# Performance work log

Measured on AMD Instinct MI355X. Metric: run time of the kernel, lower is better.

The kernel has to match this reference:

```python
import jax, jax.numpy as jnp
import numpy as np

D = 128            # actual_dim
DM = 2 * D         # d_model = 256
DI = 2 * DM        # support-encoder inner dim = 512
H = 2 * DM         # LSTMCell hidden = 512
NUM_SYMBOLS = 200000
KNN_K = 10
PROCESS_STEPS = 4
BQ, BS, NN = 4096, 128, 64


def setup_inputs() -> dict:
    key = jax.random.key(0)
    ks = jax.random.split(key, 20)
    ri = lambda k, shape, hi: jax.random.randint(k, shape, 0, hi)
    rn = lambda k, shape, s=0.05: jax.random.normal(k, shape, jnp.float32) * s
    emb = rn(ks[0], (NUM_SYMBOLS + 1, D), 0.1).at[NUM_SYMBOLS].set(0.0)  # padding row
    return {
        "query": ri(ks[1], (BQ, 2), NUM_SYMBOLS),
        "support": ri(ks[2], (BS, 2), NUM_SYMBOLS),
        "q_l_conn": ri(ks[3], (BQ, NN, 2), NUM_SYMBOLS),
        "q_l_deg": ri(ks[4], (BQ,), NN),
        "q_r_conn": ri(ks[5], (BQ, NN, 2), NUM_SYMBOLS),
        "q_r_deg": ri(ks[6], (BQ,), NN),
        "s_l_conn": ri(ks[7], (BS, NN, 2), NUM_SYMBOLS),
        "s_l_deg": ri(ks[8], (BS,), NN),
        "s_r_conn": ri(ks[9], (BS, NN, 2), NUM_SYMBOLS),
        "s_r_deg": ri(ks[10], (BS,), NN),
        "emb": emb,
        "gcn_W": rn(ks[11], (D, 2 * D)),
        "gcn_wb": jnp.zeros((D,), jnp.float32),
        "gcn_b": jnp.zeros((D,), jnp.float32),
        "se_w1": rn(ks[12], (DI, DM)),
        "se_b1": jnp.zeros((DI,), jnp.float32),
        "se_w2": rn(ks[13], (DM, DI)),
        "se_b2": jnp.zeros((DM,), jnp.float32),
        "ln_g": jnp.ones((DM,), jnp.float32),
        "ln_b": jnp.zeros((DM,), jnp.float32),
        "W_ih": rn(ks[14], (4 * H, DM)),
        "W_hh": rn(ks[15], (4 * H, H)),
        "b_ih": jnp.zeros((4 * H,), jnp.float32),
        "b_hh": jnp.zeros((4 * H,), jnp.float32),
    }


def _cos(a, b, eps=1e-8):
    num = jnp.sum(a * b, -1)
    den = jnp.maximum(jnp.linalg.norm(a, axis=-1), eps) * jnp.maximum(jnp.linalg.norm(b, axis=-1), eps)
    return num / den


def _neighbor_encoder(emb, gcn_W, gcn_wb, gcn_b, conn, ent_ids):
    rel = emb[conn[..., 0]]                     # [B,N,D]
    ent = emb[conn[..., 1]]                     # [B,N,D]
    center = emb[ent_ids][:, None, :]           # [B,1,D]
    sim = _cos(center, ent)                     # [B,N]
    _, idx = jax.lax.top_k(sim, KNN_K)          # [B,K]
    rel_k = jnp.take_along_axis(rel, idx[..., None], axis=1)
    ent_k = jnp.take_along_axis(ent, idx[..., None], axis=1)
    cat = jnp.concatenate([rel_k, ent_k], -1)   # [B,K,2D]
    h = jnp.einsum('bkf,df->bkd', cat, gcn_W) + gcn_wb + gcn_b
    return jnp.tanh(h.mean(axis=1))             # [B,D]


def _support_encoder(x, w1, b1, w2, b2, g, b):
    # residual FFN + LayerNorm (GMatching SupportEncoder), dropout off (eval)
    out = jax.nn.relu(x @ w1.T + b1) @ w2.T + b2
    y = out + x
    mu = y.mean(-1, keepdims=True)
    var = ((y - mu) ** 2).mean(-1, keepdims=True)
    return (y - mu) / jnp.sqrt(var + 1e-5) * g + b


def _query_encoder(support, query, W_ih, W_hh, b_ih, b_hh):
    # GMatching attentive LSTM process block. support: [1,DM], query: [B,DM]
    B = query.shape[0]
    h_r = jnp.zeros((B, H), query.dtype)
    c = jnp.zeros((B, H), query.dtype)
    h = query
    for _ in range(PROCESS_STEPS):
        gates = query @ W_ih.T + b_ih + h_r @ W_hh.T + b_hh
        i, f, g_, o = jnp.split(gates, 4, axis=-1)  # torch LSTMCell gate order
        c = jax.nn.sigmoid(f) * c + jax.nn.sigmoid(i) * jnp.tanh(g_)
        h_new = jax.nn.sigmoid(o) * jnp.tanh(c)     # [B,H]
        h = query + h_new[:, :DM]                   # [B,DM]
        attn = jax.nn.softmax(h @ support.T, axis=1)  # [B,1]
        r = attn @ support                          # [B,DM]
        h_r = jnp.concatenate([h, r], axis=1)       # [B,H]
    return h


def reference(query, support, q_l_conn, q_l_deg, q_r_conn, q_r_deg,
              s_l_conn, s_l_deg, s_r_conn, s_r_deg,
              emb, gcn_W, gcn_wb, gcn_b,
              se_w1, se_b1, se_w2, se_b2, ln_g, ln_b,
              W_ih, W_hh, b_ih, b_hh):
    ne = lambda conn, ids: _neighbor_encoder(emb, gcn_W, gcn_wb, gcn_b, conn, ids)
    q_nb = jnp.concatenate([ne(q_l_conn, query[:, 0]), ne(q_r_conn, query[:, 1])], -1)    # [BQ,DM]
    s_nb = jnp.concatenate([ne(s_l_conn, support[:, 0]), ne(s_r_conn, support[:, 1])], -1)  # [BS,DM]
    se = lambda x: _support_encoder(x, se_w1, se_b1, se_w2, se_b2, ln_g, ln_b)
    support_g = se(s_nb).mean(axis=0, keepdims=True)  # [1,DM]
    query_g = se(q_nb)                                # [BQ,DM]
    qf = _query_encoder(support_g, query_g, W_ih, W_hh, b_ih, b_hh)
    l2 = lambda x: x / jnp.maximum(jnp.linalg.norm(x, axis=-1, keepdims=True), 1e-12)
    return (l2(qf) @ l2(support_g).T).squeeze(-1)     # [BQ]
```

## Files before the change

kernel.cpp:

```cpp
#include <hip/hip_runtime.h>
#include <hip/hip_bf16.h>

#define D   128
#define DM  256
#define DI  512
#define HH  512
#define KNN 10
#define NN  64
#define BQ  4096
#define BS  128
#define BM2 (BQ + BS)
#define G2  1024
#define GK  256
#define NSYM 200000
#define NEB (BQ * 2 + BS * 2)
#define BKT 64
#define LDP (BKT + 8)

__device__ __forceinline__ float sigmoidf_(float x) {
    return 1.f / (1.f + __expf(-x));
}
__device__ __forceinline__ float tanh_fast(float x) {
    x = fminf(fmaxf(x, -20.f), 20.f);
    float e = __expf(2.f * x);
    return (e - 1.f) / (e + 1.f);
}
__device__ __forceinline__ ushort f2bf(float x) {
    union { float f; unsigned u; } v; v.f = x;
    unsigned r = (v.u + 0x7fffu + ((v.u >> 16) & 1u)) >> 16;
    return (ushort)r;
}

typedef __bf16  bf16x8  __attribute__((ext_vector_type(8)));
typedef float   floatx4 __attribute__((ext_vector_type(4)));

__global__ __launch_bounds__(256) void ne_prep_kernel(
    const int* __restrict__ q_l, const int* __restrict__ q_r,
    const int* __restrict__ q_ids,
    const int* __restrict__ s_l, const int* __restrict__ s_r,
    const int* __restrict__ s_ids,
    const float* __restrict__ emb,
    float* __restrict__ catm_out,
    const float* __restrict__ W_ih, const float* __restrict__ W_hh,
    const float* __restrict__ b_ih, const float* __restrict__ b_hh,
    const float* __restrict__ se_w1, const float* __restrict__ se_w2,
    ushort* __restrict__ wih_bf, ushort* __restrict__ whh_bf,
    float* __restrict__ bsumP, ushort* __restrict__ w1_bf,
    ushort* __restrict__ w2_bf)
{
    int bid = blockIdx.x;
    int tid = threadIdx.x;

    if (bid >= NEB) {
        int pb = bid - NEB;
        if (pb < G2) {
            int n = pb;
            int bn = n >> 7, r = n & 127;
            int half = (r >> 6) & 1, j = (r >> 4) & 3, l = r & 15;
            int u = bn * 32 + half * 16 + l;
            int oldrow = j * 512 + u;
            wih_bf[n * 256 + tid] = f2bf(W_ih[(size_t)oldrow * DM + tid]);
            whh_bf[n * 256 + tid] = f2bf(W_hh[(size_t)oldrow * HH + tid]);
            if (tid == 0) bsumP[n] = b_ih[oldrow] + b_hh[oldrow];
        } else {
            int idx = (pb - G2) * 256 + tid;
            w1_bf[idx] = f2bf(se_w1[idx]);
            w2_bf[idx] = f2bf(se_w2[idx]);
        }
        return;
    }

    const int *conn_l, *conn_r, *ids;
    int row;
    if (bid < BQ * 2) { conn_l = q_l; conn_r = q_r; ids = q_ids; row = bid >> 1; }
    else { conn_l = s_l; conn_r = s_r; ids = s_ids; row = (bid - BQ * 2) >> 1; }
    int side = bid & 1;
    const int* conn = (side ? conn_r : conn_l) + (size_t)row * NN * 2;
    int cid = ids[row * 2 + side];

    __shared__ int   connb[NN * 2];
    __shared__ float sim[NN];
    __shared__ int   selr[KNN], sele[KNN];

    int wave = tid >> 6, lane = tid & 63;
    int grp = lane >> 4, l16 = lane & 15;

    if (tid < NN * 2) connb[tid] = conn[tid];
    const float* cp = &emb[(size_t)cid * D + l16 * 8];
    float4 c4a = *(const float4*)cp;
    float4 c4b = *(const float4*)(cp + 4);
    float cs = c4a.x * c4a.x + c4a.y * c4a.y + c4a.z * c4a.z + c4a.w * c4a.w
             + c4b.x * c4b.x + c4b.y * c4b.y + c4b.z * c4b.z + c4b.w * c4b.w;
    #pragma unroll
    for (int off = 8; off; off >>= 1) cs += __shfl_xor(cs, off);
    float cnorm = fmaxf(sqrtf(cs), 1e-8f);
    __syncthreads();

    float4 ea[4], eb[4];
    #pragma unroll
    for (int b = 0; b < 4; b++) {
        int j = wave * 16 + b * 4 + grp;
        int eid = connb[j * 2 + 1];
        const float* ep = &emb[(size_t)eid * D + l16 * 8];
        ea[b] = *(const float4*)ep;
        eb[b] = *(const float4*)(ep + 4);
    }
    #pragma unroll
    for (int b = 0; b < 4; b++) {
        int j = wave * 16 + b * 4 + grp;
        float dot = c4a.x * ea[b].x + c4a.y * ea[b].y + c4a.z * ea[b].z + c4a.w * ea[b].w
                  + c4b.x * eb[b].x + c4b.y * eb[b].y + c4b.z * eb[b].z + c4b.w * eb[b].w;
        float ee  = ea[b].x * ea[b].x + ea[b].y * ea[b].y + ea[b].z * ea[b].z + ea[b].w * ea[b].w
                  + eb[b].x * eb[b].x + eb[b].y * eb[b].y + eb[b].z * eb[b].z + eb[b].w * eb[b].w;
        #pragma unroll
        for (int off = 8; off; off >>= 1) {
            dot += __shfl_xor(dot, off);
            ee  += __shfl_xor(ee, off);
        }
        if (l16 == 0) sim[j] = dot / (cnorm * fmaxf(sqrtf(ee), 1e-8f));
    }
    __syncthreads();

    if (wave == 0) {
        float s = sim[lane];
        int id = lane;
        for (int k = 0; k < KNN; k++) {
            float bs = s; int bi = id;
            #pragma unroll
            for (int off = 32; off; off >>= 1) {
                float os = __shfl_xor(bs, off);
                int   oi = __shfl_xor(bi, off);
                if (os > bs || (os == bs && oi < bi)) { bs = os; bi = oi; }
            }
            if (lane == 0) { selr[k] = connb[bi * 2]; sele[k] = connb[bi * 2 + 1]; }
            if (id == bi) s = -__builtin_inff();
        }
    }
    __syncthreads();

    float acc = 0.f;
    if (tid < D) {
        #pragma unroll
        for (int k = 0; k < KNN; k++) acc += emb[(size_t)selr[k] * D + tid];
    } else {
        int d = tid - D;
        #pragma unroll
        for (int k = 0; k < KNN; k++) acc += emb[(size_t)sele[k] * D + d];
    }
    catm_out[(size_t)bid * DM + tid] = acc * (1.f / KNN);
}

#define GR 16
__global__ __launch_bounds__(256) void gcn_kernel(
    const float* __restrict__ catm, const float* __restrict__ gcn_W,
    const float* __restrict__ gcn_wb, const float* __restrict__ gcn_b,
    float* __restrict__ out, ushort* __restrict__ out_bf)
{
    __shared__ float cs[GR][DM];
    __shared__ float pp[GR][DM];
    int tid = threadIdx.x;
    int m0 = blockIdx.x * GR;
    #pragma unroll
    for (int t = 0; t < 4; t++) {
        int chunk = tid + 256 * t;
        int r = chunk >> 6, c4 = chunk & 63;
        *(float4*)&cs[r][c4 * 4] = *(const float4*)&catm[(size_t)(m0 + r) * DM + c4 * 4];
    }
    __syncthreads();

    int d = tid & 127, half = tid >> 7;
    float a[GR];
    #pragma unroll
    for (int r = 0; r < GR; r++) a[r] = 0.f;
    const float4* W4 = (const float4*)(gcn_W + (size_t)d * DM + half * D);
    for (int f4 = 0; f4 < D / 4; ++f4) {
        float4 w = W4[f4];
        #pragma unroll
        for (int r = 0; r < GR; r++) {
            const float* c = &cs[r][half * D + f4 * 4];
            a[r] += w.x * c[0] + w.y * c[1] + w.z * c[2] + w.w * c[3];
        }
    }
    #pragma unroll
    for (int r = 0; r < GR; r++) pp[r][tid] = a[r];
    __syncthreads();
    if (tid < D) {
        #pragma unroll
        for (int r = 0; r < GR; r++) {
            float h = pp[r][tid] + pp[r][tid + D] + gcn_wb[tid] + gcn_b[tid];
            float th = tanh_fast(h);
            out[(size_t)(m0 + r) * D + tid] = th;
            out_bf[(size_t)(m0 + r) * D + tid] = f2bf(th);
        }
    }
}

#define GEMM64_VARS()                                                         \
    __shared__ __align__(16) ushort As[64][LDP];                              \
    __shared__ __align__(16) ushort Bs[128][LDP];                             \
    int tid = threadIdx.x;                                                    \
    int wave = tid >> 6, lane = tid & 63;                                     \
    int quad = lane >> 4, l16 = lane & 15;                                    \
    int wm = (wave >> 1) * 32, wn = (wave & 1) * 64;

#define GEMM64_CORE(AP, BP, KDIM)                                             \
    floatx4 acc[2][4];                                                        \
    _Pragma("unroll")                                                         \
    for (int i = 0; i < 2; i++)                                               \
        _Pragma("unroll")                                                     \
        for (int j = 0; j < 4; j++) acc[i][j] = (floatx4){0.f, 0.f, 0.f, 0.f};\
    for (int k0 = 0; k0 < (KDIM); k0 += BKT) {                                \
        __syncthreads();                                                      \
        _Pragma("unroll")                                                     \
        for (int t = 0; t < 2; t++) {                                         \
            int ch = t * 256 + tid;                                           \
            int r = ch >> 3, c8 = (ch & 7) * 8;                               \
            *(uint4*)&As[r][c8] = *(const uint4*)&(AP)[(size_t)(bm * 64 + r) * (KDIM) + k0 + c8]; \
        }                                                                     \
        _Pragma("unroll")                                                     \
        for (int t = 0; t < 4; t++) {                                         \
            int ch = t * 256 + tid;                                           \
            int r = ch >> 3, c8 = (ch & 7) * 8;                               \
            *(uint4*)&Bs[r][c8] = *(const uint4*)&(BP)[(size_t)(bn * 128 + r) * (KDIM) + k0 + c8]; \
        }                                                                     \
        __syncthreads();                                                      \
        _Pragma("unroll")                                                     \
        for (int kk = 0; kk < BKT; kk += 32) {                                \
            bf16x8 af[2], bv[4];                                              \
            _Pragma("unroll")                                                 \
            for (int i = 0; i < 2; i++)                                       \
                af[i] = *(const bf16x8*)&As[wm + i * 16 + l16][kk + quad * 8];\
            _Pragma("unroll")                                                 \
            for (int j = 0; j < 4; j++)                                       \
                bv[j] = *(const bf16x8*)&Bs[wn + j * 16 + l16][kk + quad * 8];\
            _Pragma("unroll")                                                 \
            for (int i = 0; i < 2; i++)                                       \
                _Pragma("unroll")                                             \
                for (int j = 0; j < 4; j++)                                   \
                    acc[i][j] = __builtin_amdgcn_mfma_f32_16x16x32_bf16(      \
                        af[i], bv[j], acc[i][j], 0, 0, 0);                    \
        }                                                                     \
    }

__global__ __launch_bounds__(256) void se_gemm1_kernel(
    const ushort* __restrict__ A, const ushort* __restrict__ B,
    const float* __restrict__ b1, ushort* __restrict__ Cbf)
{
    GEMM64_VARS();
    int bm = blockIdx.x, bn = blockIdx.y;
    GEMM64_CORE(A, B, DM);
    #pragma unroll
    for (int i = 0; i < 2; i++) {
        #pragma unroll
        for (int j = 0; j < 4; j++) {
            int row = bm * 64 + wm + i * 16 + quad * 4;
            int col = bn * 128 + wn + j * 16 + l16;
            float bb = b1[col];
            #pragma unroll
            for (int rr = 0; rr < 4; rr++)
                Cbf[(size_t)(row + rr) * DI + col] = f2bf(fmaxf(acc[i][j][rr] + bb, 0.f));
        }
    }
}

__global__ __launch_bounds__(256) void se_gemm2_kernel(
    const ushort* __restrict__ A, const ushort* __restrict__ B,
    const float* __restrict__ b2, const float* __restrict__ xres,
    float* __restrict__ C)
{
    GEMM64_VARS();
    int bm = blockIdx.x, bn = blockIdx.y;
    GEMM64_CORE(A, B, DI);
    #pragma unroll
    for (int i = 0; i < 2; i++) {
        #pragma unroll
        for (int j = 0; j < 4; j++) {
            int row = bm * 64 + wm + i * 16 + quad * 4;
            int col = bn * 128 + wn + j * 16 + l16;
            float bb = b2[col];
            #pragma unroll
            for (int rr = 0; rr < 4; rr++)
                C[(size_t)(row + rr) * DM + col] =
                    acc[i][j][rr] + bb + xres[(size_t)(row + rr) * DM + col];
        }
    }
}

#define LN_ROWS 8
__global__ __launch_bounds__(256) void ln_kernel(
    const float* __restrict__ ys, const float* __restrict__ g,
    const float* __restrict__ b, float* __restrict__ outf,
    ushort* __restrict__ outbf)
{
    int tid = threadIdx.x;
    int wave = tid >> 6, lane = tid & 63;
    int r0 = blockIdx.x * LN_ROWS;
    for (int rr = 0; rr < 2; ++rr) {
        int r = r0 + wave * 2 + rr;
        float vals[4];
        float s = 0.f;
        #pragma unroll
        for (int e = 0; e < 4; e++) {
            vals[e] = ys[(size_t)r * DM + e * 64 + lane];
            s += vals[e];
        }
        #pragma unroll
        for (int off = 32; off; off >>= 1) s += __shfl_xor(s, off);
        float mu = s * (1.f / DM);
        float v = 0.f;
        #pragma unroll
        for (int e = 0; e < 4; e++) { float dd = vals[e] - mu; v += dd * dd; }
        #pragma unroll
        for (int off = 32; off; off >>= 1) v += __shfl_xor(v, off);
        float rstd = rsqrtf(v * (1.f / DM) + 1e-5f);
        #pragma unroll
        for (int e = 0; e < 4; e++) {
            int dd = e * 64 + lane;
            float ov = (vals[e] - mu) * rstd * g[dd] + b[dd];
            outf[(size_t)r * DM + dd] = ov;
            outbf[(size_t)r * DM + dd] = f2bf(ov);
        }
    }
}

__global__ __launch_bounds__(256) void lstm_gemm0_sgw_kernel(
    const ushort* __restrict__ A, const ushort* __restrict__ B,
    const float* __restrict__ bsumP, const float* __restrict__ lnf,
    float* __restrict__ P0f, float* __restrict__ Cf, ushort* __restrict__ h_out,
    const float* __restrict__ W_hh, const float* __restrict__ b_ih,
    const float* __restrict__ b_hh, float* __restrict__ sg,
    float* __restrict__ gaddP)
{
    if (blockIdx.x >= 512) {
        __shared__ float s[DM];
        int tid = threadIdx.x;
        int sb = blockIdx.x - 512;
        float a = 0.f;
        for (int r = 0; r < BS; r++) a += lnf[(size_t)(BQ + r) * DM + tid];
        a *= (1.f / BS);
        s[tid] = a;
        if (sb == 0) sg[tid] = a;
        __syncthreads();

        int idx = sb * 256 + tid;
        int g = idx >> 8, u = idx & 255;
        int oldrow = g * 512 + u;
        const float4* w4 = (const float4*)(W_hh + (size_t)oldrow * HH + DM);
        float acc = 0.f;
        for (int f4 = 0; f4 < DM / 4; ++f4) {
            float4 w = w4[f4];
            acc += w.x * s[f4 * 4] + w.y * s[f4 * 4 + 1] + w.z * s[f4 * 4 + 2] + w.w * s[f4 * 4 + 3];
        }
        float bs = b_ih[oldrow] + b_hh[oldrow];
        int n = (u >> 5) * 128 + ((u >> 4) & 1) * 64 + g * 16 + (u & 15);
        gaddP[n] = bs + acc;
        return;
    }

    GEMM64_VARS();
    int bm = blockIdx.x >> 3, bn = blockIdx.x & 7;
    GEMM64_CORE(A, B, GK);
    int u = bn * 32 + (wn ? 16 : 0) + l16;
    size_t tile = (size_t)bm * 8 + bn;
    float b4[4];
    #pragma unroll
    for (int j = 0; j < 4; j++) b4[j] = bsumP[bn * 128 + wn + j * 16 + l16];
    #pragma unroll
    for (int i = 0; i < 2; i++) {
        int row = bm * 64 + wm + i * 16 + quad * 4;
        #pragma unroll
        for (int j = 0; j < 4; j++)
            *(floatx4*)&P0f[((tile * 8 + i * 4 + j) * 256 + tid) * 4] = acc[i][j];
        floatx4 cv4;
        #pragma unroll
        for (int rr = 0; rr < 4; rr++) {
            float iv = acc[i][0][rr] + b4[0];
            float gv = acc[i][2][rr] + b4[2];
            float ov = acc[i][3][rr] + b4[3];
            float cv = sigmoidf_(iv) * tanh_fast(gv);
            cv4[rr] = cv;
            float h = lnf[(size_t)(row + rr) * DM + u] + sigmoidf_(ov) * tanh_fast(cv);
            h_out[(size_t)(row + rr) * DM + u] = f2bf(h);
        }
        *(floatx4*)&Cf[((tile * 2 + i) * 256 + tid) * 4] = cv4;
    }
}

__global__ __launch_bounds__(256) void lstm_step_kernel(
    const ushort* __restrict__ A, const ushort* __restrict__ B,
    const float* __restrict__ P0f, const float* __restrict__ gaddP,
    const float* __restrict__ lnf, float* __restrict__ Cf,
    ushort* __restrict__ h_out, float* __restrict__ hf_out, int last)
{
    GEMM64_VARS();
    int bm = blockIdx.x, bn = blockIdx.y;
    GEMM64_CORE(A, B, GK);
    int u = bn * 32 + (wn ? 16 : 0) + l16;
    size_t tile = (size_t)bm * 8 + bn;
    float g4[4];
    #pragma unroll
    for (int j = 0; j < 4; j++) g4[j] = gaddP[bn * 128 + wn + j * 16 + l16];
    #pragma unroll
    for (int i = 0; i < 2; i++) {
        int row = bm * 64 + wm + i * 16 + quad * 4;
        floatx4 p0[4];
        #pragma unroll
        for (int j = 0; j < 4; j++)
            p0[j] = *(const floatx4*)&P0f[((tile * 8 + i * 4 + j) * 256 + tid) * 4];
        floatx4 cprev = *(const floatx4*)&Cf[((tile * 2 + i) * 256 + tid) * 4];
        floatx4 cnew;
        #pragma unroll
        for (int rr = 0; rr < 4; rr++) {
            float iv = acc[i][0][rr] + p0[0][rr] + g4[0];
            float fv = acc[i][1][rr] + p0[1][rr] + g4[1];
            float gv = acc[i][2][rr] + p0[2][rr] + g4[2];
            float ov = acc[i][3][rr] + p0[3][rr] + g4[3];
            float cv = sigmoidf_(fv) * cprev[rr] + sigmoidf_(iv) * tanh_fast(gv);
            cnew[rr] = cv;
            float h = lnf[(size_t)(row + rr) * DM + u] + sigmoidf_(ov) * tanh_fast(cv);
            if (last) hf_out[(size_t)(row + rr) * DM + u] = h;
            else      h_out[(size_t)(row + rr) * DM + u] = f2bf(h);
        }
        *(floatx4*)&Cf[((tile * 2 + i) * 256 + tid) * 4] = cnew;
    }
}

__global__ __launch_bounds__(256) void final_kernel(
    const float* __restrict__ h_ws, const float* __restrict__ sg,
    float* __restrict__ outp)
{
    __shared__ float sgs[DM];
    int tid = threadIdx.x;
    sgs[tid] = sg[tid];
    __syncthreads();
    int wave = tid >> 6, lane = tid & 63;
    float sn = 0.f;
    #pragma unroll
    for (int e = 0; e < 4; e++) { float v = sgs[e * 64 + lane]; sn += v * v; }
    #pragma unroll
    for (int off = 32; off; off >>= 1) sn += __shfl_xor(sn, off);
    float sgnorm = fmaxf(sqrtf(sn), 1e-12f);

    int row = blockIdx.x * 4 + wave;
    const float* h = h_ws + (size_t)row * DM;
    float dot = 0.f, hn = 0.f;
    #pragma unroll
    for (int e = 0; e < 4; e++) {
        float hv = h[e * 64 + lane];
        dot += hv * sgs[e * 64 + lane];
        hn += hv * hv;
    }
    #pragma unroll
    for (int off = 32; off; off >>= 1) { dot += __shfl_xor(dot, off); hn += __shfl_xor(hn, off); }
    if (lane == 0) outp[row] = dot / (fmaxf(sqrtf(hn), 1e-12f) * sgnorm);
}

extern "C" void kernel_launch(void* const* d_in, const int* in_sizes, int n_in,
                              void* d_out, int out_size, void* d_ws, size_t ws_size,
                              hipStream_t stream)
{
    const int* query    = (const int*)d_in[0];
    const int* support  = (const int*)d_in[1];
    const int* q_l_conn = (const int*)d_in[2];
    const int* q_r_conn = (const int*)d_in[4];
    const int* s_l_conn = (const int*)d_in[6];
    const int* s_r_conn = (const int*)d_in[8];
    const float* emb    = (const float*)d_in[10];
    const float* gcn_W  = (const float*)d_in[11];
    const float* gcn_wb = (const float*)d_in[12];
    const float* gcn_b  = (const float*)d_in[13];
    const float* se_w1  = (const float*)d_in[14];
    const float* se_b1  = (const float*)d_in[15];
    const float* se_w2  = (const float*)d_in[16];
    const float* se_b2  = (const float*)d_in[17];
    const float* ln_g   = (const float*)d_in[18];
    const float* ln_b   = (const float*)d_in[19];
    const float* W_ih   = (const float*)d_in[20];
    const float* W_hh   = (const float*)d_in[21];
    const float* b_ih   = (const float*)d_in[22];
    const float* b_hh   = (const float*)d_in[23];
    float* out = (float*)d_out;

    char* wsb = (char*)d_ws;
    float*  xf     = (float*)wsb;  wsb += (size_t)BM2 * DM * 4;
    ushort* xb     = (ushort*)wsb; wsb += (size_t)BM2 * DM * 2;
    ushort* t1_bf  = (ushort*)wsb; wsb += (size_t)BM2 * DI * 2;
    float*  ys     = (float*)wsb;  wsb += (size_t)BM2 * DM * 4;
    float*  ln_f   = (float*)wsb;  wsb += (size_t)BM2 * DM * 4;
    ushort* ln_bf  = (ushort*)wsb; wsb += (size_t)BM2 * DM * 2;
    float*  sg     = (float*)wsb;  wsb += DM * 4;
    float*  bsumP  = (float*)wsb;  wsb += G2 * 4;
    float*  gaddP  = (float*)wsb;  wsb += G2 * 4;
    ushort* wih_bf = (ushort*)wsb; wsb += (size_t)G2 * DM * 2;
    ushort* whh_bf = (ushort*)wsb; wsb += (size_t)G2 * DM * 2;
    ushort* w1_bf  = (ushort*)wsb; wsb += (size_t)DI * DM * 2;
    ushort* w2_bf  = (ushort*)wsb; wsb += (size_t)DM * DI * 2;
    float*  P0f    = (float*)wsb;  wsb += (size_t)BQ * G2 * 4;
    float*  Cf     = (float*)wsb;  wsb += (size_t)BQ * DM * 4;
    ushort* h_bfA  = (ushort*)wsb; wsb += (size_t)BQ * DM * 2;
    ushort* h_bfB  = (ushort*)wsb; wsb += (size_t)BQ * DM * 2;
    float*  h_f    = (float*)wsb;  wsb += (size_t)BQ * DM * 4;

    float* catm = P0f;

    ne_prep_kernel<<<NEB + G2 + 512, 256, 0, stream>>>(
        q_l_conn, q_r_conn, query, s_l_conn, s_r_conn, support,
        emb, catm,
        W_ih, W_hh, b_ih, b_hh, se_w1, se_w2,
        wih_bf, whh_bf, bsumP, w1_bf, w2_bf);
    gcn_kernel<<<(BM2 * 2) / GR, 256, 0, stream>>>(catm, gcn_W, gcn_wb, gcn_b,
                                                   xf, xb);
    { dim3 g1(BM2 / 64, DI / 128);
      se_gemm1_kernel<<<g1, 256, 0, stream>>>(xb, w1_bf, se_b1, t1_bf); }
    { dim3 g2(BM2 / 64, DM / 128);
      se_gemm2_kernel<<<g2, 256, 0, stream>>>(t1_bf, w2_bf, se_b2, xf, ys); }
    ln_kernel<<<BM2 / LN_ROWS, 256, 0, stream>>>(ys, ln_g, ln_b, ln_f, ln_bf);

    lstm_gemm0_sgw_kernel<<<516, 256, 0, stream>>>(
        ln_bf, wih_bf, bsumP, ln_f, P0f, Cf, h_bfA,
        W_hh, b_ih, b_hh, sg, gaddP);

    dim3 ggrid(BQ / 64, G2 / 128);
    lstm_step_kernel<<<ggrid, 256, 0, stream>>>(h_bfA, whh_bf, P0f, gaddP, ln_f,
                                                Cf, h_bfB, h_f, 0);
    lstm_step_kernel<<<ggrid, 256, 0, stream>>>(h_bfB, whh_bf, P0f, gaddP, ln_f,
                                                Cf, h_bfA, h_f, 0);
    lstm_step_kernel<<<ggrid, 256, 0, stream>>>(h_bfA, whh_bf, P0f, gaddP, ln_f,
                                                Cf, h_bfB, h_f, 1);
    final_kernel<<<BQ / 4, 256, 0, stream>>>(h_f, sg, out);
}
```

Measured before the change: 335.6 us.

## Recompute input projection in LSTM steps via concatenated weights instead of storing P0

Instead of writing the fp32 input-gate projection P0 (BQ x 1024 floats) once and reading it back in every LSTM step, each step now runs a K=512 GEMM over the concatenated [ln, h] input against a combined bf16 W_ih|W_hh matrix. All MFMA GEMMs also drop from 64-row to 32-row tiles, doubling grid sizes for more parallelism. This trades extra MFMA work per step for removing heavy fp32 P0 traffic, and the smaller tiles lower per-block reuse of the B operand.

```diff
diff --git a/kernel.cpp b/kernel.cpp
--- a/kernel.cpp
+++ b/kernel.cpp
@@ -44,7 +44,7 @@
     const float* __restrict__ W_ih, const float* __restrict__ W_hh,
     const float* __restrict__ b_ih, const float* __restrict__ b_hh,
     const float* __restrict__ se_w1, const float* __restrict__ se_w2,
-    ushort* __restrict__ wih_bf, ushort* __restrict__ whh_bf,
+    ushort* __restrict__ wcomb,
     float* __restrict__ bsumP, ushort* __restrict__ w1_bf,
     ushort* __restrict__ w2_bf)
 {
@@ -59,8 +59,8 @@
             int half = (r >> 6) & 1, j = (r >> 4) & 3, l = r & 15;
             int u = bn * 32 + half * 16 + l;
             int oldrow = j * 512 + u;
-            wih_bf[n * 256 + tid] = f2bf(W_ih[(size_t)oldrow * DM + tid]);
-            whh_bf[n * 256 + tid] = f2bf(W_hh[(size_t)oldrow * HH + tid]);
+            wcomb[(size_t)n * 512 + tid]       = f2bf(W_ih[(size_t)oldrow * DM + tid]);
+            wcomb[(size_t)n * 512 + 256 + tid] = f2bf(W_hh[(size_t)oldrow * HH + tid]);
             if (tid == 0) bsumP[n] = b_ih[oldrow] + b_hh[oldrow];
         } else {
             int idx = (pb - G2) * 256 + tid;
@@ -195,50 +195,42 @@
     }
 }
 
-#define GEMM64_VARS()                                                         \
-    __shared__ __align__(16) ushort As[64][LDP];                              \
+#define GEMM32_VARS()                                                         \
+    __shared__ __align__(16) ushort As[32][LDP];                              \
     __shared__ __align__(16) ushort Bs[128][LDP];                             \
     int tid = threadIdx.x;                                                    \
     int wave = tid >> 6, lane = tid & 63;                                     \
     int quad = lane >> 4, l16 = lane & 15;                                    \
-    int wm = (wave >> 1) * 32, wn = (wave & 1) * 64;
-
-#define GEMM64_CORE(AP, BP, KDIM)                                             \
-    floatx4 acc[2][4];                                                        \
+    int wm = (wave >> 1) * 16, wn = (wave & 1) * 64;
+
+#define GEMM32_CORE(AP, ASTRIDE, BP, BSTRIDE, KDIM)                           \
+    floatx4 acc[4];                                                           \
     _Pragma("unroll")                                                         \
-    for (int i = 0; i < 2; i++)                                               \
-        _Pragma("unroll")                                                     \
-        for (int j = 0; j < 4; j++) acc[i][j] = (floatx4){0.f, 0.f, 0.f, 0.f};\
+    for (int j = 0; j < 4; j++) acc[j] = (floatx4){0.f, 0.f, 0.f, 0.f};       \
     for (int k0 = 0; k0 < (KDIM); k0 += BKT) {                                \
         __syncthreads();                                                      \
-        _Pragma("unroll")                                                     \
-        for (int t = 0; t < 2; t++) {                                         \
-            int ch = t * 256 + tid;                                           \
-            int r = ch >> 3, c8 = (ch & 7) * 8;                               \
-            *(uint4*)&As[r][c8] = *(const uint4*)&(AP)[(size_t)(bm * 64 + r) * (KDIM) + k0 + c8]; \
+        {                                                                     \
+            int r = tid >> 3, c8 = (tid & 7) * 8;                             \
+            *(uint4*)&As[r][c8] = *(const uint4*)&(AP)[(size_t)(bm * 32 + r) * (ASTRIDE) + k0 + c8]; \
         }                                                                     \
         _Pragma("unroll")                                                     \
         for (int t = 0; t < 4; t++) {                                         \
             int ch = t * 256 + tid;                                           \
             int r = ch >> 3, c8 = (ch & 7) * 8;                               \
-            *(uint4*)&Bs[r][c8] = *(const uint4*)&(BP)[(size_t)(bn * 128 + r) * (KDIM) + k0 + c8]; \
+            *(uint4*)&Bs[r][c8] = *(const uint4*)&(BP)[(size_t)(bn * 128 + r) * (BSTRIDE) + k0 + c8]; \
         }                                                                     \
         __syncthreads();                                                      \
         _Pragma("unroll")                                                     \
         for (int kk = 0; kk < BKT; kk += 32) {                                \
-            bf16x8 af[2], bv[4];                                              \
-            _Pragma("unroll")                                                 \
-            for (int i = 0; i < 2; i++)                                       \
-                af[i] = *(const bf16x8*)&As[wm + i * 16 + l16][kk + quad * 8];\
+            bf16x8 af, bv[4];                                                 \
+            af = *(const bf16x8*)&As[wm + l16][kk + quad * 8];                \
             _Pragma("unroll")                                                 \
             for (int j = 0; j < 4; j++)                                       \
                 bv[j] = *(const bf16x8*)&Bs[wn + j * 16 + l16][kk + quad * 8];\
             _Pragma("unroll")                                                 \
-            for (int i = 0; i < 2; i++)                                       \
-                _Pragma("unroll")                                             \
-                for (int j = 0; j < 4; j++)                                   \
-                    acc[i][j] = __builtin_amdgcn_mfma_f32_16x16x32_bf16(      \
-                        af[i], bv[j], acc[i][j], 0, 0, 0);                    \
+            for (int j = 0; j < 4; j++)                                       \
+                acc[j] = __builtin_amdgcn_mfma_f32_16x16x32_bf16(             \
+                    af, bv[j], acc[j], 0, 0, 0);                              \
         }                                                                     \
     }
 
@@ -246,20 +238,17 @@
     const ushort* __restrict__ A, const ushort* __restrict__ B,
     const float* __restrict__ b1, ushort* __restrict__ Cbf)
 {
-    GEMM64_VARS();
+    GEMM32_VARS();
     int bm = blockIdx.x, bn = blockIdx.y;
-    GEMM64_CORE(A, B, DM);
-    #pragma unroll
-    for (int i = 0; i < 2; i++) {
-        #pragma unroll
-        for (int j = 0; j < 4; j++) {
-            int row = bm * 64 + wm + i * 16 + quad * 4;
-            int col = bn * 128 + wn + j * 16 + l16;
-            float bb = b1[col];
-            #pragma unroll
-            for (int rr = 0; rr < 4; rr++)
-                Cbf[(size_t)(row + rr) * DI + col] = f2bf(fmaxf(acc[i][j][rr] + bb, 0.f));
-        }
+    GEMM32_CORE(A, DM, B, DM, DM);
+    #pragma unroll
+    for (int j = 0; j < 4; j++) {
+        int row = bm * 32 + wm + quad * 4;
+        int col = bn * 128 + wn + j * 16 + l16;
+        float bb = b1[col];
+        #pragma unroll
+        for (int rr = 0; rr < 4; rr++)
+            Cbf[(size_t)(row + rr) * DI + col] = f2bf(fmaxf(acc[j][rr] + bb, 0.f));
     }
 }
 
@@ -268,21 +257,18 @@
     const float* __restrict__ b2, const float* __restrict__ xres,
     float* __restrict__ C)
 {
-    GEMM64_VARS();
+    GEMM32_VARS();
     int bm = blockIdx.x, bn = blockIdx.y;
-    GEMM64_CORE(A, B, DI);
-    #pragma unroll
-    for (int i = 0; i < 2; i++) {
-        #pragma unroll
-        for (int j = 0; j < 4; j++) {
-            int row = bm * 64 + wm + i * 16 + quad * 4;
-            int col = bn * 128 + wn + j * 16 + l16;
-            float bb = b2[col];
-            #pragma unroll
-            for (int rr = 0; rr < 4; rr++)
-                C[(size_t)(row + rr) * DM + col] =
-                    acc[i][j][rr] + bb + xres[(size_t)(row + rr) * DM + col];
-        }
+    GEMM32_CORE(A, DI, B, DI, DI);
+    #pragma unroll
+    for (int j = 0; j < 4; j++) {
+        int row = bm * 32 + wm + quad * 4;
+        int col = bn * 128 + wn + j * 16 + l16;
+        float bb = b2[col];
+        #pragma unroll
+        for (int rr = 0; rr < 4; rr++)
+            C[(size_t)(row + rr) * DM + col] =
+                acc[j][rr] + bb + xres[(size_t)(row + rr) * DM + col];
     }
 }
 
@@ -324,17 +310,17 @@
 }
 
 __global__ __launch_bounds__(256) void lstm_gemm0_sgw_kernel(
-    const ushort* __restrict__ A, const ushort* __restrict__ B,
+    const ushort* __restrict__ A, const ushort* __restrict__ wcomb,
     const float* __restrict__ bsumP, const float* __restrict__ lnf,
-    float* __restrict__ P0f, float* __restrict__ Cf, ushort* __restrict__ h_out,
+    float* __restrict__ Cf, ushort* __restrict__ h_out,
     const float* __restrict__ W_hh, const float* __restrict__ b_ih,
     const float* __restrict__ b_hh, float* __restrict__ sg,
     float* __restrict__ gaddP)
 {
-    if (blockIdx.x >= 512) {
+    if (blockIdx.x >= 1024) {
         __shared__ float s[DM];
         int tid = threadIdx.x;
-        int sb = blockIdx.x - 512;
+        int sb = blockIdx.x - 1024;
         float a = 0.f;
         for (int r = 0; r < BS; r++) a += lnf[(size_t)(BQ + r) * DM + tid];
         a *= (1.f / BS);
@@ -357,71 +343,91 @@
         return;
     }
 
-    GEMM64_VARS();
+    GEMM32_VARS();
     int bm = blockIdx.x >> 3, bn = blockIdx.x & 7;
-    GEMM64_CORE(A, B, GK);
+    GEMM32_CORE(A, GK, wcomb, 512, GK);
     int u = bn * 32 + (wn ? 16 : 0) + l16;
     size_t tile = (size_t)bm * 8 + bn;
     float b4[4];
     #pragma unroll
     for (int j = 0; j < 4; j++) b4[j] = bsumP[bn * 128 + wn + j * 16 + l16];
-    #pragma unroll
-    for (int i = 0; i < 2; i++) {
-        int row = bm * 64 + wm + i * 16 + quad * 4;
-        #pragma unroll
-        for (int j = 0; j < 4; j++)
-            *(floatx4*)&P0f[((tile * 8 + i * 4 + j) * 256 + tid) * 4] = acc[i][j];
+    {
+        int row = bm * 32 + wm + quad * 4;
         floatx4 cv4;
         #pragma unroll
         for (int rr = 0; rr < 4; rr++) {
-            float iv = acc[i][0][rr] + b4[0];
-            float gv = acc[i][2][rr] + b4[2];
-            float ov = acc[i][3][rr] + b4[3];
+            float iv = acc[0][rr] + b4[0];
+            float gv = acc[2][rr] + b4[2];
+            float ov = acc[3][rr] + b4[3];
             float cv = sigmoidf_(iv) * tanh_fast(gv);
             cv4[rr] = cv;
             float h = lnf[(size_t)(row + rr) * DM + u] + sigmoidf_(ov) * tanh_fast(cv);
             h_out[(size_t)(row + rr) * DM + u] = f2bf(h);
         }
-        *(floatx4*)&Cf[((tile * 2 + i) * 256 + tid) * 4] = cv4;
+        *(floatx4*)&Cf[(tile * 256 + tid) * 4] = cv4;
     }
 }
 
 __global__ __launch_bounds__(256) void lstm_step_kernel(
-    const ushort* __restrict__ A, const ushort* __restrict__ B,
-    const float* __restrict__ P0f, const float* __restrict__ gaddP,
+    const ushort* __restrict__ lnbf, const ushort* __restrict__ hin,
+    const ushort* __restrict__ wcomb, const float* __restrict__ gaddP,
     const float* __restrict__ lnf, float* __restrict__ Cf,
     ushort* __restrict__ h_out, float* __restrict__ hf_out, int last)
 {
-    GEMM64_VARS();
+    GEMM32_VARS();
     int bm = blockIdx.x, bn = blockIdx.y;
-    GEMM64_CORE(A, B, GK);
+    floatx4 acc[4];
+    #pragma unroll
+    for (int j = 0; j < 4; j++) acc[j] = (floatx4){0.f, 0.f, 0.f, 0.f};
+    for (int k0 = 0; k0 < 512; k0 += BKT) {
+        const ushort* Abase = (k0 < 256) ? (lnbf + k0) : (hin + (k0 - 256));
+        __syncthreads();
+        {
+            int r = tid >> 3, c8 = (tid & 7) * 8;
+            *(uint4*)&As[r][c8] = *(const uint4*)&Abase[(size_t)(bm * 32 + r) * 256 + c8];
+        }
+        #pragma unroll
+        for (int t = 0; t < 4; t++) {
+            int ch = t * 256 + tid;
+            int r = ch >> 3, c8 = (ch & 7) * 8;
+            *(uint4*)&Bs[r][c8] = *(const uint4*)&wcomb[(size_t)(bn * 128 + r) * 512 + k0 + c8];
+        }
+        __syncthreads();
+        #pragma unroll
+        for (int kk = 0; kk < BKT; kk += 32) {
+            bf16x8 af, bv[4];
+            af = *(const bf16x8*)&As[wm + l16][kk + quad * 8];
+            #pragma unroll
+            for (int j = 0; j < 4; j++)
+                bv[j] = *(const bf16x8*)&Bs[wn + j * 16 + l16][kk + quad * 8];
+            #pragma unroll
+            for (int j = 0; j < 4; j++)
+                acc[j] = __builtin_amdgcn_mfma_f32_16x16x32_bf16(
+                    af, bv[j], acc[j], 0, 0, 0);
+        }
+    }
     int u = bn * 32 + (wn ? 16 : 0) + l16;
     size_t tile = (size_t)bm * 8 + bn;
     float g4[4];
     #pragma unroll
     for (int j = 0; j < 4; j++) g4[j] = gaddP[bn * 128 + wn + j * 16 + l16];
-    #pragma unroll
-    for (int i = 0; i < 2; i++) {
-        int row = bm * 64 + wm + i * 16 + quad * 4;
-        floatx4 p0[4];
-        #pragma unroll
-        for (int j = 0; j < 4; j++)
-            p0[j] = *(const floatx4*)&P0f[((tile * 8 + i * 4 + j) * 256 + tid) * 4];
-        floatx4 cprev = *(const floatx4*)&Cf[((tile * 2 + i) * 256 + tid) * 4];
+    {
+        int row = bm * 32 + wm + quad * 4;
+        floatx4 cprev = *(const floatx4*)&Cf[(tile * 256 + tid) * 4];
         floatx4 cnew;
         #pragma unroll
         for (int rr = 0; rr < 4; rr++) {
-            float iv = acc[i][0][rr] + p0[0][rr] + g4[0];
-            float fv = acc[i][1][rr] + p0[1][rr] + g4[1];
-            float gv = acc[i][2][rr] + p0[2][rr] + g4[2];
-            float ov = acc[i][3][rr] + p0[3][rr] + g4[3];
+            float iv = acc[0][rr] + g4[0];
+            float fv = acc[1][rr] + g4[1];
+            float gv = acc[2][rr] + g4[2];
+            float ov = acc[3][rr] + g4[3];
             float cv = sigmoidf_(fv) * cprev[rr] + sigmoidf_(iv) * tanh_fast(gv);
             cnew[rr] = cv;
             float h = lnf[(size_t)(row + rr) * DM + u] + sigmoidf_(ov) * tanh_fast(cv);
             if (last) hf_out[(size_t)(row + rr) * DM + u] = h;
             else      h_out[(size_t)(row + rr) * DM + u] = f2bf(h);
         }
-        *(floatx4*)&Cf[((tile * 2 + i) * 256 + tid) * 4] = cnew;
+        *(floatx4*)&Cf[(tile * 256 + tid) * 4] = cnew;
     }
 }
 
@@ -491,41 +497,38 @@
     float*  sg     = (float*)wsb;  wsb += DM * 4;
     float*  bsumP  = (float*)wsb;  wsb += G2 * 4;
     float*  gaddP  = (float*)wsb;  wsb += G2 * 4;
-    ushort* wih_bf = (ushort*)wsb; wsb += (size_t)G2 * DM * 2;
-    ushort* whh_bf = (ushort*)wsb; wsb += (size_t)G2 * DM * 2;
+    ushort* wcomb  = (ushort*)wsb; wsb += (size_t)G2 * 512 * 2;
     ushort* w1_bf  = (ushort*)wsb; wsb += (size_t)DI * DM * 2;
     ushort* w2_bf  = (ushort*)wsb; wsb += (size_t)DM * DI * 2;
-    float*  P0f    = (float*)wsb;  wsb += (size_t)BQ * G2 * 4;
+    float*  catm   = (float*)wsb;  wsb += (size_t)NEB * DM * 4;
     float*  Cf     = (float*)wsb;  wsb += (size_t)BQ * DM * 4;
     ushort* h_bfA  = (ushort*)wsb; wsb += (size_t)BQ * DM * 2;
     ushort* h_bfB  = (ushort*)wsb; wsb += (size_t)BQ * DM * 2;
     float*  h_f    = (float*)wsb;  wsb += (size_t)BQ * DM * 4;
 
-    float* catm = P0f;
-
     ne_prep_kernel<<<NEB + G2 + 512, 256, 0, stream>>>(
         q_l_conn, q_r_conn, query, s_l_conn, s_r_conn, support,
         emb, catm,
         W_ih, W_hh, b_ih, b_hh, se_w1, se_w2,
-        wih_bf, whh_bf, bsumP, w1_bf, w2_bf);
+        wcomb, bsumP, w1_bf, w2_bf);
     gcn_kernel<<<(BM2 * 2) / GR, 256, 0, stream>>>(catm, gcn_W, gcn_wb, gcn_b,
                                                    xf, xb);
-    { dim3 g1(BM2 / 64, DI / 128);
+    { dim3 g1(BM2 / 32, DI / 128);
       se_gemm1_kernel<<<g1, 256, 0, stream>>>(xb, w1_bf, se_b1, t1_bf); }
-    { dim3 g2(BM2 / 64, DM / 128);
+    { dim3 g2(BM2 / 32, DM / 128);
       se_gemm2_kernel<<<g2, 256, 0, stream>>>(t1_bf, w2_bf, se_b2, xf, ys); }
     ln_kernel<<<BM2 / LN_ROWS, 256, 0, stream>>>(ys, ln_g, ln_b, ln_f, ln_bf);
 
-    lstm_gemm0_sgw_kernel<<<516, 256, 0, stream>>>(
-        ln_bf, wih_bf, bsumP, ln_f, P0f, Cf, h_bfA,
+    lstm_gemm0_sgw_kernel<<<1028, 256, 0, stream>>>(
+        ln_bf, wcomb, bsumP, ln_f, Cf, h_bfA,
         W_hh, b_ih, b_hh, sg, gaddP);
 
-    dim3 ggrid(BQ / 64, G2 / 128);
-    lstm_step_kernel<<<ggrid, 256, 0, stream>>>(h_bfA, whh_bf, P0f, gaddP, ln_f,
+    dim3 ggrid(BQ / 32, G2 / 128);
+    lstm_step_kernel<<<ggrid, 256, 0, stream>>>(ln_bf, h_bfA, wcomb, gaddP, ln_f,
                                                 Cf, h_bfB, h_f, 0);
-    lstm_step_kernel<<<ggrid, 256, 0, stream>>>(h_bfB, whh_bf, P0f, gaddP, ln_f,
+    lstm_step_kernel<<<ggrid, 256, 0, stream>>>(ln_bf, h_bfB, wcomb, gaddP, ln_f,
                                                 Cf, h_bfA, h_f, 0);
-    lstm_step_kernel<<<ggrid, 256, 0, stream>>>(h_bfA, whh_bf, P0f, gaddP, ln_f,
+    lstm_step_kernel<<<ggrid, 256, 0, stream>>>(ln_bf, h_bfA, wcomb, gaddP, ln_f,
                                                 Cf, h_bfB, h_f, 1);
     final_kernel<<<BQ / 4, 256, 0, stream>>>(h_f, sg, out);
 }
```

Result: slower. 353.6 us (+5.3%).
